# Performance work log

Hardware: AMD Instinct MI355X
Metric: run time of the kernel (lower is better)

## Reference

```python
import math
import jax, jax.numpy as jnp
import numpy as np

B, T, C, H = 2, 1024, 1024, 16
D = C // H
BASE_SCALE = 0.03125
ATTN_ALPHA_INIT, MLP_ALPHA_INIT = 0.05, 0.05


def sinusoidal_embeddings(n, d):
    pos = jnp.arange(n, dtype=jnp.float32)[:, None]
    div = jnp.exp(jnp.arange(0, d, 2, dtype=jnp.float32) * (-math.log(10000.0) / d))
    emb = jnp.zeros((n, d), dtype=jnp.float32)
    emb = emb.at[:, 0::2].set(jnp.sin(pos * div))
    emb = emb.at[:, 1::2].set(jnp.cos(pos * div))
    return emb


def apply_rope(pos, q):
    # pos: (T, D); q: (B, H, T, D). Faithful to source: returns only the rotated-scaled component.
    pos = pos[-q.shape[2]:]
    d = q.shape[-1]
    sin, cos = pos[:, : d // 2], pos[:, d // 2 :]
    q_rot = jnp.stack((-q[..., 1::2], q[..., ::2]), axis=-1)  # (B,H,T,D/2,2)
    sc = jnp.stack((cos, sin), axis=-1)  # (T, D/2, 2)
    return (q_rot * sc).reshape(q.shape)


def justnorm(x):
    return x / jnp.linalg.norm(x, axis=-1, keepdims=True)


def setup_inputs() -> dict:
    key = jax.random.key(0)
    ks = jax.random.split(key, 14)
    w = lambda k, shape: jax.random.normal(k, shape, jnp.float32) * 0.02
    return {
        "h": jax.random.normal(ks[0], (B, T, C), jnp.float32),
        "Wq": w(ks[1], (C, C)),
        "Wk": w(ks[2], (C, C)),
        "Wv": w(ks[3], (C, C)),
        "Wo": w(ks[4], (C, C)),
        "Wfc": w(ks[5], (8 * C, C)),
        "Wproj": w(ks[6], (C, 4 * C)),
        "sqk": BASE_SCALE * jnp.ones(C) + w(ks[7], (C,)) * 0.05,
        "suv": jnp.ones(8 * C) + w(ks[8], (8 * C,)) * 0.05,
        "attn_alpha": BASE_SCALE * jnp.ones(C) + w(ks[9], (C,)) * 0.05,
        "mlp_alpha": BASE_SCALE * jnp.ones(C) + w(ks[10], (C,)) * 0.05,
        "thr_c": 1.6 * jnp.ones(H) + w(ks[11], (H,)) * 0.5,
        "stp": 10.0 * jnp.ones(H),
    }


def reference(h, Wq, Wk, Wv, Wo, Wfc, Wproj, sqk, suv, attn_alpha, mlp_alpha, thr_c, stp):
    softmax_scale = math.sqrt(D)  # nGPT uses sqrt(head_dim) since q,k are unit-normalized

    # --- attention branch (no pre-norm in nGPT mode) ---
    q = (h @ Wq.T).reshape(B, T, H, D).transpose(0, 2, 1, 3)  # (B,H,T,D)
    k = (h @ Wk.T).reshape(B, T, H, D).transpose(0, 2, 1, 3)
    v = (h @ Wv.T).reshape(B, T, H, D).transpose(0, 2, 1, 3)

    pos = sinusoidal_embeddings(T, D)
    q = apply_rope(pos, q)
    k = apply_rope(pos, k)

    sqk_s = (sqk * (1.0 / BASE_SCALE)).reshape(1, H, 1, D)
    q = sqk_s * justnorm(q)
    k = sqk_s * justnorm(k)

    scores = jnp.einsum("bhqd,bhkd->bhqk", q, k) * softmax_scale  # (B,H,T,T)
    causal = jnp.tril(jnp.ones((T, T), dtype=bool))
    w = jax.nn.softmax(jnp.where(causal, scores, -1e9), axis=-1)
    # soft score threshold: per-head sigmoid gate on raw scores, then renormalize
    gate = jax.nn.sigmoid(stp[None, :, None, None] * (scores - thr_c[None, :, None, None]))
    w = w * gate
    w = w / jnp.sum(w, axis=-1, keepdims=True)

    y = jnp.einsum("bhqk,bhkd->bhqd", w, v).transpose(0, 2, 1, 3).reshape(B, T, C)
    h_att = y @ Wo.T

    lr = jnp.abs(attn_alpha * (ATTN_ALPHA_INIT / BASE_SCALE))
    A = justnorm(h)
    Bn = justnorm(h_att)
    h = justnorm(A + lr * (Bn - A))

    # --- MLP branch ---
    uv = h @ Wfc.T  # (B,T,8C)
    uv = (suv * math.sqrt(C)) * uv
    u, vv = jnp.split(uv, 2, axis=-1)
    x_mlp = u * (vv * jax.nn.sigmoid(vv))
    h_mlp = x_mlp @ Wproj.T

    lr2 = jnp.abs(mlp_alpha * (MLP_ALPHA_INIT / BASE_SCALE))
    A = justnorm(h)
    Bn = justnorm(h_mlp)
    h = justnorm(A + lr2 * (Bn - A))
    return h
```

## Files before the change

kernel.cpp:

```cpp
#include <hip/hip_runtime.h>
#include <hip/hip_bf16.h>
#include <math.h>

typedef _Float16 f16x8 __attribute__((ext_vector_type(8)));
typedef float f32x4 __attribute__((ext_vector_type(4)));
typedef float f32x2 __attribute__((ext_vector_type(2)));
typedef unsigned short u16;
typedef unsigned int u32;
typedef u16 u16x4 __attribute__((ext_vector_type(4)));
typedef u16 u16x8 __attribute__((ext_vector_type(8)));

#define DEVI static __device__ __forceinline__
#define LDSS 72
#define MB (1u << 20)

DEVI u16 f2h(float f) {
    _Float16 h = (_Float16)f;
    return __builtin_bit_cast(u16, h);
}
DEVI float h2f(u16 u) {
    return (float)__builtin_bit_cast(_Float16, u);
}
DEVI f32x4 mfma16(f16x8 a, f16x8 b, f32x4 c) {
    return __builtin_amdgcn_mfma_f32_16x16x32_f16(a, b, c, 0, 0, 0);
}
DEVI void gload16(const u16* g, u16* l) {
    __builtin_amdgcn_global_load_lds((const __attribute__((address_space(1))) void*)g,
                                     (__attribute__((address_space(3))) void*)l, 16, 0, 0);
}

DEVI void stage128(const u16* __restrict__ g, size_t row0, int ldg, int k0, u16* lds) {
    int t = threadIdx.x;
    const u16* src = g + (row0 + (size_t)(t >> 3)) * (size_t)ldg + k0 + (t & 7) * 8;
    u16* dst = lds + (t >> 6) * 512;
#pragma unroll
    for (int is = 0; is < 4; is++)
        gload16(src + (size_t)is * 32 * ldg, dst + is * 2048);
}

DEVI void gemm128_core(const u16* __restrict__ A, const u16* __restrict__ B,
                       int ldk, int kbeg, int kend, int m0, int n0,
                       u16* As, u16* Bs, f32x4 acc[4][4]) {
    int lane = threadIdx.x & 63, w = threadIdx.x >> 6;
    int wm = (w >> 1) * 64, wn = (w & 1) * 64;
    int lrow = lane & 15, lg = lane >> 4;
    for (int k0 = kbeg; k0 < kend; k0 += 64) {
        __syncthreads();
        stage128(A, m0, ldk, k0, As);
        stage128(B, n0, ldk, k0, Bs);
        __syncthreads();
#pragma unroll
        for (int ks = 0; ks < 2; ks++) {
            f16x8 af[4], bf[4];
#pragma unroll
            for (int i = 0; i < 4; i++) {
                af[i] = *reinterpret_cast<f16x8*>(&As[(wm + i * 16 + lrow) * 64 + ks * 32 + lg * 8]);
                bf[i] = *reinterpret_cast<f16x8*>(&Bs[(wn + i * 16 + lrow) * 64 + ks * 32 + lg * 8]);
            }
#pragma unroll
            for (int i = 0; i < 4; i++)
#pragma unroll
                for (int j = 0; j < 4; j++)
                    acc[i][j] = mfma16(af[i], bf[j], acc[i][j]);
        }
    }
}

__global__ void cvt_kernel(const float* __restrict__ h, const float* __restrict__ Wq,
                           const float* __restrict__ Wk, const float* __restrict__ Wv,
                           const float* __restrict__ Wo, const float* __restrict__ Wfc,
                           const float* __restrict__ Wproj, u16* __restrict__ dst) {
    int bid = blockIdx.x;
    const float* src;
    size_t doff;
    int sb;
    if (bid < 1024)      { src = h;     sb = 0;    doff = 0; }
    else if (bid < 1536) { src = Wq;    sb = 1024; doff = 2097152; }
    else if (bid < 2048) { src = Wk;    sb = 1536; doff = 3145728; }
    else if (bid < 2560) { src = Wv;    sb = 2048; doff = 4194304; }
    else if (bid < 3072) { src = Wo;    sb = 2560; doff = 5242880; }
    else if (bid < 7168) { src = Wfc;   sb = 3072; doff = 10485760; }
    else                 { src = Wproj; sb = 7168; doff = 6291456; }
    size_t idx = (size_t)(bid - sb) * 2048 + threadIdx.x * 8;
    f32x4 a = *reinterpret_cast<const f32x4*>(src + idx);
    f32x4 b = *reinterpret_cast<const f32x4*>(src + idx + 4);
    u16x8 o;
    o[0] = f2h(a[0]); o[1] = f2h(a[1]); o[2] = f2h(a[2]); o[3] = f2h(a[3]);
    o[4] = f2h(b[0]); o[5] = f2h(b[1]); o[6] = f2h(b[2]); o[7] = f2h(b[3]);
    *reinterpret_cast<u16x8*>(dst + doff + idx) = o;
}

__global__ __launch_bounds__(256, 2) void qkv_h_kernel(
    const u16* __restrict__ hb, const u16* __restrict__ Wqh, const u16* __restrict__ Wkh,
    const u16* __restrict__ Wvh, u16* __restrict__ qb, u16* __restrict__ kb, u16* __restrict__ vb) {
    __shared__ u16 As[128 * 64];
    __shared__ u16 Bs[128 * 64];
    int z = blockIdx.z;
    const u16* W = (z == 0) ? Wqh : (z == 1) ? Wkh : Wvh;
    u16* dst = (z == 0) ? qb : (z == 1) ? kb : vb;
    int m0 = blockIdx.y * 128, n0 = blockIdx.x * 128;
    f32x4 acc[4][4];
    f32x4 zf = {0.f, 0.f, 0.f, 0.f};
#pragma unroll
    for (int i = 0; i < 4; i++)
#pragma unroll
        for (int j = 0; j < 4; j++) acc[i][j] = zf;
    gemm128_core(hb, W, 1024, 0, 1024, m0, n0, As, Bs, acc);
    int lane = threadIdx.x & 63, w = threadIdx.x >> 6;
    int wm = (w >> 1) * 64, wn = (w & 1) * 64;
    int lrow = lane & 15, lg = lane >> 4;
#pragma unroll
    for (int i = 0; i < 4; i++)
#pragma unroll
        for (int j = 0; j < 4; j++)
#pragma unroll
            for (int r = 0; r < 4; r++) {
                int m = m0 + wm + i * 16 + lg * 4 + r;
                int n = n0 + wn + j * 16 + lrow;
                dst[(size_t)m * 1024 + n] = f2h(acc[i][j][r]);
            }
}

__global__ __launch_bounds__(256, 2) void gemm_h_kernel(
    const u16* __restrict__ A, const u16* __restrict__ B, u16* __restrict__ out,
    int ldk, int ksplit, int osplit, int N) {
    __shared__ u16 As[128 * 64];
    __shared__ u16 Bs[128 * 64];
    int z = blockIdx.z;
    int m0 = blockIdx.y * 128, n0 = blockIdx.x * 128;
    f32x4 acc[4][4];
    f32x4 zf = {0.f, 0.f, 0.f, 0.f};
#pragma unroll
    for (int i = 0; i < 4; i++)
#pragma unroll
        for (int j = 0; j < 4; j++) acc[i][j] = zf;
    gemm128_core(A, B, ldk, z * ksplit, (z + 1) * ksplit, m0, n0, As, Bs, acc);
    u16* o = out + (size_t)z * osplit;
    int lane = threadIdx.x & 63, w = threadIdx.x >> 6;
    int wm = (w >> 1) * 64, wn = (w & 1) * 64;
    int lrow = lane & 15, lg = lane >> 4;
#pragma unroll
    for (int i = 0; i < 4; i++)
#pragma unroll
        for (int j = 0; j < 4; j++)
#pragma unroll
            for (int r = 0; r < 4; r++) {
                int m = m0 + wm + i * 16 + lg * 4 + r;
                int n = n0 + wn + j * 16 + lrow;
                o[(size_t)m * N + n] = f2h(acc[i][j][r]);
            }
}

__global__ void qkprep_kernel(u16* __restrict__ qb, u16* __restrict__ kb,
                              const float* __restrict__ sqk) {
    u16* buf = blockIdx.z ? kb : qb;
    int pair = blockIdx.x * 4 + (threadIdx.x >> 6);
    int m = pair >> 4, hh = pair & 15;
    int tt = m & 1023;
    int d = threadIdx.x & 63;
    size_t off = (size_t)m * 1024 + hh * 64 + d;
    float x = h2f(buf[off]);
    float xn = __shfl_xor(x, 1);
    int j = (d & 1) ? ((d - 1) >> 1) : (32 + (d >> 1));
    float dv = exp2f(-(float)(j >> 1) * 0.41524101186092029f);
    float ang = (float)tt * dv;
    float e = (j & 1) ? cosf(ang) : sinf(ang);
    float xr = (d & 1) ? (xn * e) : (-xn * e);
    float ss = xr * xr;
#pragma unroll
    for (int o = 1; o < 64; o <<= 1) ss += __shfl_xor(ss, o);
    float sc = rsqrtf(ss) * sqk[hh * 64 + d] * 32.0f;
    buf[off] = f2h(xr * sc);
}

__global__ __launch_bounds__(128) void attn_kernel(
    const u16* __restrict__ qb, const u16* __restrict__ kb, const u16* __restrict__ vb,
    const float* __restrict__ thr_c, const float* __restrict__ stp,
    u16* __restrict__ yph, f32x2* __restrict__ mden) {
    const int T = 1024, C = 1024;
    int qt = 31 - (blockIdx.x >> 2);
    int c = blockIdx.x & 3;
    int bh = blockIdx.y;
    int b = bh >> 4, hh = bh & 15;
    int q0 = qt * 32;
    int nkt = (q0 >> 6) + 1;
    __shared__ u16 Vt[2][64 * LDSS];
    __shared__ u16 Ps[32 * LDSS];
    int t = threadIdx.x;
    int lane = t & 63, w = t >> 6;
    int lrow = lane & 15, lg = lane >> 4, lk = lg * 8;
    int kvp = t & 31, db = t >> 5;

    const u16* qrowp = qb + (size_t)(b * T + q0 + w * 16 + lrow) * C + hh * 64;
    f16x8 qfr[2];
    qfr[0] = *reinterpret_cast<const f16x8*>(qrowp + lk);
    qfr[1] = *reinterpret_cast<const f16x8*>(qrowp + 32 + lk);

    float thr = thr_c[hh], st = stp[hh];
    float stthr = st * thr;
    float mrun = -1e30f, den = 0.f;
    f32x4 yacc[4];
    f32x4 zf = {0.f, 0.f, 0.f, 0.f};
#pragma unroll
    for (int i = 0; i < 4; i++) yacc[i] = zf;
    int qg = q0 + w * 16 + lrow;

    f16x8 kpre[8];
    u16x4 vr[8];
    const u16* kbase0 = kb + (size_t)(b * T + lrow) * C + hh * 64 + lk;
    const u16* vbase0 = vb + (size_t)(b * T + 2 * kvp) * C + hh * 64 + db * 16;

    if (c < nkt) {
        const u16* kbase = kbase0 + (size_t)(c << 6) * C;
        const u16* vsrc = vbase0 + (size_t)(c << 6) * C;
#pragma unroll
        for (int ks = 0; ks < 2; ks++)
#pragma unroll
            for (int f = 0; f < 4; f++)
                kpre[ks * 4 + f] = *reinterpret_cast<const f16x8*>(kbase + (size_t)(f * 16) * C + ks * 32);
#pragma unroll
        for (int dd = 0; dd < 4; dd++) {
            vr[dd * 2] = *reinterpret_cast<const u16x4*>(vsrc + dd * 4);
            vr[dd * 2 + 1] = *reinterpret_cast<const u16x4*>(vsrc + C + dd * 4);
        }
    }

    int bufsel = 0;
    for (int kt = c; kt < nkt; kt += 4) {
        int kv0 = kt << 6;
        u16* VB = Vt[bufsel];
        bufsel ^= 1;
#pragma unroll
        for (int dd = 0; dd < 4; dd++)
#pragma unroll
            for (int e = 0; e < 4; e++) {
                u32 v = (u32)vr[dd * 2][e] | ((u32)vr[dd * 2 + 1][e] << 16);
                *reinterpret_cast<u32*>(&VB[(db * 16 + dd * 4 + e) * LDSS + 2 * kvp]) = v;
            }
        f32x4 sacc[4];
#pragma unroll
        for (int f = 0; f < 4; f++) sacc[f] = zf;
#pragma unroll
        for (int ks = 0; ks < 2; ks++)
#pragma unroll
            for (int f = 0; f < 4; f++)
                sacc[f] = mfma16(kpre[ks * 4 + f], qfr[ks], sacc[f]);

        if (kt + 4 < nkt) {
            const u16* kbase = kbase0 + (size_t)((kt + 4) << 6) * C;
            const u16* vsrc = vbase0 + (size_t)((kt + 4) << 6) * C;
#pragma unroll
            for (int ks = 0; ks < 2; ks++)
#pragma unroll
                for (int f = 0; f < 4; f++)
                    kpre[ks * 4 + f] = *reinterpret_cast<const f16x8*>(kbase + (size_t)(f * 16) * C + ks * 32);
#pragma unroll
            for (int dd = 0; dd < 4; dd++) {
                vr[dd * 2] = *reinterpret_cast<const u16x4*>(vsrc + dd * 4);
                vr[dd * 2 + 1] = *reinterpret_cast<const u16x4*>(vsrc + C + dd * 4);
            }
        }

        float svv[16];
        float tmax = -1e30f;
        bool last = (kt == nkt - 1);
#pragma unroll
        for (int f = 0; f < 4; f++)
#pragma unroll
            for (int r = 0; r < 4; r++) {
                float s = sacc[f][r] * 8.0f;
                if (last) {
                    int kvg = kv0 + f * 16 + lg * 4 + r;
                    if (kvg > qg) s = -1e30f;
                }
                svv[f * 4 + r] = s;
                tmax = fmaxf(tmax, s);
            }
        tmax = fmaxf(tmax, __shfl_xor(tmax, 16));
        tmax = fmaxf(tmax, __shfl_xor(tmax, 32));
        float zM = stthr - st * tmax;
        float spM = tmax - __logf(1.0f + __expf(zM));
        float mnew = fmaxf(mrun, spM);
        float alpha = __expf(mrun - mnew);
        float tden = 0.f;
        u16 pu[16];
#pragma unroll
        for (int i = 0; i < 16; i++) {
            float s = svv[i];
            float e2 = __expf(s - mnew);
            float eg = __expf(stthr - st * s);
            float p = e2 * __builtin_amdgcn_rcpf(1.0f + eg);
            u16 ph = f2h(p);
            pu[i] = ph;
            tden += h2f(ph);
        }
        tden += __shfl_xor(tden, 16);
        tden += __shfl_xor(tden, 32);
        den = den * alpha + tden;
        mrun = mnew;

#pragma unroll
        for (int f = 0; f < 4; f++) {
            u16x4 u = {pu[f * 4 + 0], pu[f * 4 + 1], pu[f * 4 + 2], pu[f * 4 + 3]};
            *reinterpret_cast<u16x4*>(&Ps[(w * 16 + lrow) * LDSS + f * 16 + lg * 4]) = u;
        }
        float a4[4];
#pragma unroll
        for (int r = 0; r < 4; r++) a4[r] = __shfl(alpha, lg * 4 + r);
#pragma unroll
        for (int nf = 0; nf < 4; nf++)
#pragma unroll
            for (int r = 0; r < 4; r++) yacc[nf][r] *= a4[r];

        __syncthreads();

#pragma unroll
        for (int ks = 0; ks < 2; ks++) {
            f16x8 pf = *reinterpret_cast<f16x8*>(&Ps[(w * 16 + lrow) * LDSS + ks * 32 + lk]);
#pragma unroll
            for (int nf = 0; nf < 4; nf++) {
                f16x8 vf = *reinterpret_cast<f16x8*>(&VB[(nf * 16 + lrow) * LDSS + ks * 32 + lk]);
                yacc[nf] = mfma16(pf, vf, yacc[nf]);
            }
        }
    }
    u16* ypc = yph + (size_t)c * 2097152;
#pragma unroll
    for (int nf = 0; nf < 4; nf++)
#pragma unroll
        for (int r = 0; r < 4; r++) {
            int qrow = q0 + w * 16 + lg * 4 + r;
            ypc[(size_t)(b * T + qrow) * C + hh * 64 + nf * 16 + lrow] = f2h(yacc[nf][r]);
        }
    if (lg == 0) {
        f32x2 md;
        md[0] = mrun; md[1] = den;
        mden[((size_t)c * 32 + bh) * 1024 + (q0 + w * 16 + lrow)] = md;
    }
}

__global__ void attn_merge_kernel(const u16* __restrict__ yph, const f32x2* __restrict__ mden,
                                  u16* __restrict__ y) {
    int row = blockIdx.x;
    int b = row >> 10, tr = row & 1023;
    int t = threadIdx.x;
#pragma unroll
    for (int i = 0; i < 4; i++) {
        int idx = t + 256 * i;
        int hh = idx >> 6;
        float m[4], d[4];
        float M = -1e30f;
#pragma unroll
        for (int p = 0; p < 4; p++) {
            f32x2 md = mden[((size_t)p * 32 + b * 16 + hh) * 1024 + tr];
            m[p] = md[0]; d[p] = md[1];
            M = fmaxf(M, m[p]);
        }
        size_t off = (size_t)row * 1024 + idx;
        float dn = 0.f, acc = 0.f;
#pragma unroll
        for (int p = 0; p < 4; p++) {
            float wp = __expf(m[p] - M);
            dn += d[p] * wp;
            acc += h2f(yph[off + (size_t)p * 2097152]) * wp;
        }
        y[off] = f2h(acc / dn);
    }
}

__global__ __launch_bounds__(256, 2) void fc_silu_kernel(
    const u16* __restrict__ h1h, const u16* __restrict__ Wfch,
    const float* __restrict__ suv, u16* __restrict__ xmlp) {
    __shared__ u16 As[128 * 64];
    __shared__ u16 Bu[128 * 64];
    __shared__ u16 Bv[128 * 64];
    int m0 = blockIdx.y * 128, n0 = blockIdx.x * 128;
    f32x4 au[4][4], av[4][4];
    f32x4 zf = {0.f, 0.f, 0.f, 0.f};
#pragma unroll
    for (int i = 0; i < 4; i++)
#pragma unroll
        for (int j = 0; j < 4; j++) { au[i][j] = zf; av[i][j] = zf; }
    int lane = threadIdx.x & 63, w = threadIdx.x >> 6;
    int wm = (w >> 1) * 64, wn = (w & 1) * 64;
    int lrow = lane & 15, lg = lane >> 4;
    for (int k0 = 0; k0 < 1024; k0 += 64) {
        __syncthreads();
        stage128(h1h, m0, 1024, k0, As);
        stage128(Wfch, n0, 1024, k0, Bu);
        stage128(Wfch, 4096 + n0, 1024, k0, Bv);
        __syncthreads();
#pragma unroll
        for (int ks = 0; ks < 2; ks++) {
            f16x8 af[4], bu[4], bv[4];
#pragma unroll
            for (int i = 0; i < 4; i++) {
                af[i] = *reinterpret_cast<f16x8*>(&As[(wm + i * 16 + lrow) * 64 + ks * 32 + lg * 8]);
                bu[i] = *reinterpret_cast<f16x8*>(&Bu[(wn + i * 16 + lrow) * 64 + ks * 32 + lg * 8]);
                bv[i] = *reinterpret_cast<f16x8*>(&Bv[(wn + i * 16 + lrow) * 64 + ks * 32 + lg * 8]);
            }
#pragma unroll
            for (int i = 0; i < 4; i++)
#pragma unroll
                for (int j = 0; j < 4; j++) {
                    au[i][j] = mfma16(af[i], bu[j], au[i][j]);
                    av[i][j] = mfma16(af[i], bv[j], av[i][j]);
                }
        }
    }
#pragma unroll
    for (int i = 0; i < 4; i++)
#pragma unroll
        for (int j = 0; j < 4; j++) {
            int n = n0 + wn + j * 16 + lrow;
            float su = suv[n] * 32.0f;
            float sv = suv[4096 + n] * 32.0f;
#pragma unroll
            for (int r = 0; r < 4; r++) {
                int m = m0 + wm + i * 16 + lg * 4 + r;
                float uu = au[i][j][r] * su;
                float vv = av[i][j][r] * sv;
                float sig = 1.0f / (1.0f + __expf(-vv));
                xmlp[(size_t)m * 4096 + n] = f2h(uu * vv * sig);
            }
        }
}

__global__ void normres_kernel(const float* __restrict__ base, const u16* __restrict__ dparts,
                               int nparts, int pstride, const float* __restrict__ alpha,
                               float* __restrict__ outf, u16* __restrict__ outh) {
    int row = blockIdx.x;
    int t = threadIdx.x;
    const float* pb = base + (size_t)row * 1024;
    float xb[4], xd[4];
    float ssb = 0.f, ssd = 0.f;
#pragma unroll
    for (int i = 0; i < 4; i++) {
        size_t off = (size_t)row * 1024 + t + 256 * i;
        xb[i] = pb[t + 256 * i];
        float d = 0.f;
        for (int p = 0; p < nparts; p++) d += h2f(dparts[off + (size_t)p * pstride]);
        xd[i] = d;
        ssb += xb[i] * xb[i];
        ssd += xd[i] * xd[i];
    }
#pragma unroll
    for (int o = 1; o < 64; o <<= 1) { ssb += __shfl_xor(ssb, o); ssd += __shfl_xor(ssd, o); }
    __shared__ float red[8];
    int w = t >> 6;
    if ((t & 63) == 0) { red[w * 2] = ssb; red[w * 2 + 1] = ssd; }
    __syncthreads();
    ssb = red[0] + red[2] + red[4] + red[6];
    ssd = red[1] + red[3] + red[5] + red[7];
    float rb = rsqrtf(ssb), rd = rsqrtf(ssd);
    float c[4];
    float ssc = 0.f;
#pragma unroll
    for (int i = 0; i < 4; i++) {
        float a = xb[i] * rb;
        float bb = xd[i] * rd;
        float lr = fabsf(alpha[t + 256 * i] * 1.6f);
        float cv = a + lr * (bb - a);
        c[i] = cv;
        ssc += cv * cv;
    }
#pragma unroll
    for (int o = 1; o < 64; o <<= 1) ssc += __shfl_xor(ssc, o);
    __syncthreads();
    if ((t & 63) == 0) red[w] = ssc;
    __syncthreads();
    ssc = red[0] + red[1] + red[2] + red[3];
    float rc = rsqrtf(ssc);
#pragma unroll
    for (int i = 0; i < 4; i++) {
        float v = c[i] * rc;
        size_t off = (size_t)row * 1024 + t + 256 * i;
        outf[off] = v;
        if (outh) outh[off] = f2h(v);
    }
}

extern "C" void kernel_launch(void* const* d_in, const int* in_sizes, int n_in,
                              void* d_out, int out_size, void* d_ws, size_t ws_size,
                              hipStream_t stream) {
    const float* h = (const float*)d_in[0];
    const float* Wq = (const float*)d_in[1];
    const float* Wk = (const float*)d_in[2];
    const float* Wv = (const float*)d_in[3];
    const float* Wo = (const float*)d_in[4];
    const float* Wfc = (const float*)d_in[5];
    const float* Wproj = (const float*)d_in[6];
    const float* sqk = (const float*)d_in[7];
    const float* suv = (const float*)d_in[8];
    const float* attn_alpha = (const float*)d_in[9];
    const float* mlp_alpha = (const float*)d_in[10];
    const float* thr_c = (const float*)d_in[11];
    const float* stp = (const float*)d_in[12];

    char* ws = (char*)d_ws;
    u16* f16heap = (u16*)ws;
    u16* hb     = f16heap + 0;
    u16* Wqh    = f16heap + 2097152;
    u16* Wkh    = f16heap + 3145728;
    u16* Wvh    = f16heap + 4194304;
    u16* Woh    = f16heap + 5242880;
    u16* Wprojh = f16heap + 6291456;
    u16* Wfch   = f16heap + 10485760;
    u16* partsP = Wfch;
    u16* qb   = (u16*)(ws + (size_t)36 * MB);
    u16* kb   = (u16*)(ws + (size_t)40 * MB);
    u16* vb   = (u16*)(ws + (size_t)44 * MB);
    u16* y    = (u16*)(ws + (size_t)48 * MB);
    u16* yph  = (u16*)(ws + (size_t)52 * MB);
    f32x2* mden = (f32x2*)(ws + (size_t)68 * MB);
    u16* hattP = (u16*)(ws + (size_t)52 * MB);
    float* h1 = (float*)(ws + (size_t)36 * MB);
    u16* h1h  = (u16*)(ws + (size_t)44 * MB);
    u16* xmlp = (u16*)(ws + (size_t)52 * MB);
    float* out = (float*)d_out;

    cvt_kernel<<<9216, 256, 0, stream>>>(h, Wq, Wk, Wv, Wo, Wfc, Wproj, f16heap);
    qkv_h_kernel<<<dim3(8, 16, 3), 256, 0, stream>>>(hb, Wqh, Wkh, Wvh, qb, kb, vb);
    qkprep_kernel<<<dim3(8192, 1, 2), 256, 0, stream>>>(qb, kb, sqk);
    attn_kernel<<<dim3(128, 32), 128, 0, stream>>>(qb, kb, vb, thr_c, stp, yph, mden);
    attn_merge_kernel<<<2048, 256, 0, stream>>>(yph, mden, y);
    gemm_h_kernel<<<dim3(8, 16, 4), 256, 0, stream>>>(y, Woh, hattP, 1024, 256, 2097152, 1024);
    normres_kernel<<<2048, 256, 0, stream>>>(h, hattP, 4, 2097152, attn_alpha, h1, h1h);
    fc_silu_kernel<<<dim3(32, 16), 256, 0, stream>>>(h1h, Wfch, suv, xmlp);
    gemm_h_kernel<<<dim3(8, 16, 4), 256, 0, stream>>>(xmlp, Wprojh, partsP, 4096, 1024, 2097152, 1024);
    normres_kernel<<<2048, 256, 0, stream>>>(h1, partsP, 4, 2097152, mlp_alpha, out, (u16*)nullptr);
}
```

Measured before the change: 203.5 us.

## Double-buffer GEMM LDS staging and interleave Wfc rows for fc_silu

Replaces the single-buffer GEMM mainloop with a double-buffered one that issues the next K-tile's global-to-LDS loads before computing the current tile, using vmcnt waits and raw barriers. The Wfc conversion now interleaves u and v rows, so fc_silu can use the shared GEMM core with a 128-wide tile and pair the u/v accumulators via a lane shuffle. This doubles the fc_silu grid and drops its separate triple-buffer loop. The cost is twice the LDS per block, which may lower occupancy. It also relies on hand-written waitcnt values being correct.

```diff
diff --git a/kernel.cpp b/kernel.cpp
--- a/kernel.cpp
+++ b/kernel.cpp
@@ -38,24 +38,36 @@
         gload16(src + (size_t)is * 32 * ldg, dst + is * 2048);
 }
 
-DEVI void gemm128_core(const u16* __restrict__ A, const u16* __restrict__ B,
+DEVI void gemm128_dbuf(const u16* __restrict__ A, const u16* __restrict__ B,
                        int ldk, int kbeg, int kend, int m0, int n0,
-                       u16* As, u16* Bs, f32x4 acc[4][4]) {
+                       u16* As0, u16* As1, u16* Bs0, u16* Bs1, f32x4 acc[4][4]) {
     int lane = threadIdx.x & 63, w = threadIdx.x >> 6;
     int wm = (w >> 1) * 64, wn = (w & 1) * 64;
     int lrow = lane & 15, lg = lane >> 4;
-    for (int k0 = kbeg; k0 < kend; k0 += 64) {
-        __syncthreads();
-        stage128(A, m0, ldk, k0, As);
-        stage128(B, n0, ldk, k0, Bs);
-        __syncthreads();
+    int nt = (kend - kbeg) >> 6;
+    stage128(A, m0, ldk, kbeg, As0);
+    stage128(B, n0, ldk, kbeg, Bs0);
+    for (int t = 0; t < nt; t++) {
+        u16* Ac = (t & 1) ? As1 : As0;
+        u16* Bc = (t & 1) ? Bs1 : Bs0;
+        if (t + 1 < nt) {
+            u16* An = (t & 1) ? As0 : As1;
+            u16* Bn = (t & 1) ? Bs0 : Bs1;
+            stage128(A, m0, ldk, kbeg + (t + 1) * 64, An);
+            stage128(B, n0, ldk, kbeg + (t + 1) * 64, Bn);
+            asm volatile("s_waitcnt vmcnt(8)" ::: "memory");
+        } else {
+            asm volatile("s_waitcnt vmcnt(0)" ::: "memory");
+        }
+        __builtin_amdgcn_s_barrier();
+        __builtin_amdgcn_sched_barrier(0);
 #pragma unroll
         for (int ks = 0; ks < 2; ks++) {
             f16x8 af[4], bf[4];
 #pragma unroll
             for (int i = 0; i < 4; i++) {
-                af[i] = *reinterpret_cast<f16x8*>(&As[(wm + i * 16 + lrow) * 64 + ks * 32 + lg * 8]);
-                bf[i] = *reinterpret_cast<f16x8*>(&Bs[(wn + i * 16 + lrow) * 64 + ks * 32 + lg * 8]);
+                af[i] = *reinterpret_cast<f16x8*>(&Ac[(wm + i * 16 + lrow) * 64 + ks * 32 + lg * 8]);
+                bf[i] = *reinterpret_cast<f16x8*>(&Bc[(wn + i * 16 + lrow) * 64 + ks * 32 + lg * 8]);
             }
 #pragma unroll
             for (int i = 0; i < 4; i++)
@@ -63,6 +75,7 @@
                 for (int j = 0; j < 4; j++)
                     acc[i][j] = mfma16(af[i], bf[j], acc[i][j]);
         }
+        __builtin_amdgcn_s_barrier();
     }
 }
 
@@ -74,12 +87,13 @@
     const float* src;
     size_t doff;
     int sb;
+    bool ilv = false;
     if (bid < 1024)      { src = h;     sb = 0;    doff = 0; }
     else if (bid < 1536) { src = Wq;    sb = 1024; doff = 2097152; }
     else if (bid < 2048) { src = Wk;    sb = 1536; doff = 3145728; }
     else if (bid < 2560) { src = Wv;    sb = 2048; doff = 4194304; }
     else if (bid < 3072) { src = Wo;    sb = 2560; doff = 5242880; }
-    else if (bid < 7168) { src = Wfc;   sb = 3072; doff = 10485760; }
+    else if (bid < 7168) { src = Wfc;   sb = 3072; doff = 10485760; ilv = true; }
     else                 { src = Wproj; sb = 7168; doff = 6291456; }
     size_t idx = (size_t)(bid - sb) * 2048 + threadIdx.x * 8;
     f32x4 a = *reinterpret_cast<const f32x4*>(src + idx);
@@ -87,14 +101,20 @@
     u16x8 o;
     o[0] = f2h(a[0]); o[1] = f2h(a[1]); o[2] = f2h(a[2]); o[3] = f2h(a[3]);
     o[4] = f2h(b[0]); o[5] = f2h(b[1]); o[6] = f2h(b[2]); o[7] = f2h(b[3]);
-    *reinterpret_cast<u16x8*>(dst + doff + idx) = o;
+    size_t didx = idx;
+    if (ilv) {
+        size_t row = idx >> 10, col = idx & 1023;
+        size_t nrow = (row < 4096) ? (row * 2) : ((row - 4096) * 2 + 1);
+        didx = nrow * 1024 + col;
+    }
+    *reinterpret_cast<u16x8*>(dst + doff + didx) = o;
 }
 
 __global__ __launch_bounds__(256, 2) void qkv_h_kernel(
     const u16* __restrict__ hb, const u16* __restrict__ Wqh, const u16* __restrict__ Wkh,
     const u16* __restrict__ Wvh, u16* __restrict__ qb, u16* __restrict__ kb, u16* __restrict__ vb) {
-    __shared__ u16 As[128 * 64];
-    __shared__ u16 Bs[128 * 64];
+    __shared__ u16 As[2][128 * 64];
+    __shared__ u16 Bs[2][128 * 64];
     int z = blockIdx.z;
     const u16* W = (z == 0) ? Wqh : (z == 1) ? Wkh : Wvh;
     u16* dst = (z == 0) ? qb : (z == 1) ? kb : vb;
@@ -105,7 +125,7 @@
     for (int i = 0; i < 4; i++)
 #pragma unroll
         for (int j = 0; j < 4; j++) acc[i][j] = zf;
-    gemm128_core(hb, W, 1024, 0, 1024, m0, n0, As, Bs, acc);
+    gemm128_dbuf(hb, W, 1024, 0, 1024, m0, n0, As[0], As[1], Bs[0], Bs[1], acc);
     int lane = threadIdx.x & 63, w = threadIdx.x >> 6;
     int wm = (w >> 1) * 64, wn = (w & 1) * 64;
     int lrow = lane & 15, lg = lane >> 4;
@@ -124,8 +144,8 @@
 __global__ __launch_bounds__(256, 2) void gemm_h_kernel(
     const u16* __restrict__ A, const u16* __restrict__ B, u16* __restrict__ out,
     int ldk, int ksplit, int osplit, int N) {
-    __shared__ u16 As[128 * 64];
-    __shared__ u16 Bs[128 * 64];
+    __shared__ u16 As[2][128 * 64];
+    __shared__ u16 Bs[2][128 * 64];
     int z = blockIdx.z;
     int m0 = blockIdx.y * 128, n0 = blockIdx.x * 128;
     f32x4 acc[4][4];
@@ -134,7 +154,7 @@
     for (int i = 0; i < 4; i++)
 #pragma unroll
         for (int j = 0; j < 4; j++) acc[i][j] = zf;
-    gemm128_core(A, B, ldk, z * ksplit, (z + 1) * ksplit, m0, n0, As, Bs, acc);
+    gemm128_dbuf(A, B, ldk, z * ksplit, (z + 1) * ksplit, m0, n0, As[0], As[1], Bs[0], Bs[1], acc);
     u16* o = out + (size_t)z * osplit;
     int lane = threadIdx.x & 63, w = threadIdx.x >> 6;
     int wm = (w >> 1) * 64, wn = (w & 1) * 64;
@@ -369,59 +389,41 @@
 }
 
 __global__ __launch_bounds__(256, 2) void fc_silu_kernel(
-    const u16* __restrict__ h1h, const u16* __restrict__ Wfch,
+    const u16* __restrict__ h1h, const u16* __restrict__ Wfc2,
     const float* __restrict__ suv, u16* __restrict__ xmlp) {
-    __shared__ u16 As[128 * 64];
-    __shared__ u16 Bu[128 * 64];
-    __shared__ u16 Bv[128 * 64];
-    int m0 = blockIdx.y * 128, n0 = blockIdx.x * 128;
-    f32x4 au[4][4], av[4][4];
+    __shared__ u16 As[2][128 * 64];
+    __shared__ u16 Bs[2][128 * 64];
+    int m0 = blockIdx.y * 128, n0 = blockIdx.x * 64;
+    f32x4 acc[4][4];
     f32x4 zf = {0.f, 0.f, 0.f, 0.f};
 #pragma unroll
     for (int i = 0; i < 4; i++)
 #pragma unroll
-        for (int j = 0; j < 4; j++) { au[i][j] = zf; av[i][j] = zf; }
+        for (int j = 0; j < 4; j++) acc[i][j] = zf;
+    gemm128_dbuf(h1h, Wfc2, 1024, 0, 1024, m0, 2 * n0, As[0], As[1], Bs[0], Bs[1], acc);
     int lane = threadIdx.x & 63, w = threadIdx.x >> 6;
     int wm = (w >> 1) * 64, wn = (w & 1) * 64;
     int lrow = lane & 15, lg = lane >> 4;
-    for (int k0 = 0; k0 < 1024; k0 += 64) {
-        __syncthreads();
-        stage128(h1h, m0, 1024, k0, As);
-        stage128(Wfch, n0, 1024, k0, Bu);
-        stage128(Wfch, 4096 + n0, 1024, k0, Bv);
-        __syncthreads();
-#pragma unroll
-        for (int ks = 0; ks < 2; ks++) {
-            f16x8 af[4], bu[4], bv[4];
-#pragma unroll
-            for (int i = 0; i < 4; i++) {
-                af[i] = *reinterpret_cast<f16x8*>(&As[(wm + i * 16 + lrow) * 64 + ks * 32 + lg * 8]);
-                bu[i] = *reinterpret_cast<f16x8*>(&Bu[(wn + i * 16 + lrow) * 64 + ks * 32 + lg * 8]);
-                bv[i] = *reinterpret_cast<f16x8*>(&Bv[(wn + i * 16 + lrow) * 64 + ks * 32 + lg * 8]);
-            }
-#pragma unroll
-            for (int i = 0; i < 4; i++)
-#pragma unroll
-                for (int j = 0; j < 4; j++) {
-                    au[i][j] = mfma16(af[i], bu[j], au[i][j]);
-                    av[i][j] = mfma16(af[i], bv[j], av[i][j]);
-                }
-        }
-    }
 #pragma unroll
     for (int i = 0; i < 4; i++)
 #pragma unroll
         for (int j = 0; j < 4; j++) {
-            int n = n0 + wn + j * 16 + lrow;
+            int bn = wn + j * 16 + lrow;
+            int n = n0 + (bn >> 1);
+            bool isu = (bn & 1) == 0;
             float su = suv[n] * 32.0f;
             float sv = suv[4096 + n] * 32.0f;
 #pragma unroll
             for (int r = 0; r < 4; r++) {
-                int m = m0 + wm + i * 16 + lg * 4 + r;
-                float uu = au[i][j][r] * su;
-                float vv = av[i][j][r] * sv;
+                float own = acc[i][j][r];
+                float other = __shfl_xor(own, 1);
+                float uu = (isu ? own : other) * su;
+                float vv = (isu ? other : own) * sv;
                 float sig = 1.0f / (1.0f + __expf(-vv));
-                xmlp[(size_t)m * 4096 + n] = f2h(uu * vv * sig);
+                if (isu) {
+                    int m = m0 + wm + i * 16 + lg * 4 + r;
+                    xmlp[(size_t)m * 4096 + n] = f2h(uu * vv * sig);
+                }
             }
         }
 }
@@ -505,8 +507,8 @@
     u16* Wvh    = f16heap + 4194304;
     u16* Woh    = f16heap + 5242880;
     u16* Wprojh = f16heap + 6291456;
-    u16* Wfch   = f16heap + 10485760;
-    u16* partsP = Wfch;
+    u16* Wfc2   = f16heap + 10485760;
+    u16* partsP = Wfc2;
     u16* qb   = (u16*)(ws + (size_t)36 * MB);
     u16* kb   = (u16*)(ws + (size_t)40 * MB);
     u16* vb   = (u16*)(ws + (size_t)44 * MB);
@@ -526,7 +528,7 @@
     attn_merge_kernel<<<2048, 256, 0, stream>>>(yph, mden, y);
     gemm_h_kernel<<<dim3(8, 16, 4), 256, 0, stream>>>(y, Woh, hattP, 1024, 256, 2097152, 1024);
     normres_kernel<<<2048, 256, 0, stream>>>(h, hattP, 4, 2097152, attn_alpha, h1, h1h);
-    fc_silu_kernel<<<dim3(32, 16), 256, 0, stream>>>(h1h, Wfch, suv, xmlp);
+    fc_silu_kernel<<<dim3(64, 16), 256, 0, stream>>>(h1h, Wfc2, suv, xmlp);
     gemm_h_kernel<<<dim3(8, 16, 4), 256, 0, stream>>>(xmlp, Wprojh, partsP, 4096, 1024, 2097152, 1024);
     normres_kernel<<<2048, 256, 0, stream>>>(h1, partsP, 4, 2097152, mlp_alpha, out, (u16*)nullptr);
 }
```

Result: slower. 221.5 us (+8.8%).

## Fuse RoPE and QK normalization into QKV GEMM epilogue; raise MFMA priority

Applied to the files above, without the earlier changes.

Moves the rotary embedding and per-head L2 normalization with sqk scaling into the epilogue of the QKV projection GEMM. Each wave owns a 64-wide head slice, so the per-row sum of squares is reduced across lanes with shuffles inside the wave. This drops the separate qkprep kernel, its extra read and write of the q and k buffers, and one launch. It also wraps the attention MFMA sections in s_setprio to favor the matrix-issue phases, at the cost of more transcendental work in the GEMM epilogue.

```diff
diff --git a/kernel.cpp b/kernel.cpp
--- a/kernel.cpp
+++ b/kernel.cpp
@@ -92,7 +92,8 @@
 
 __global__ __launch_bounds__(256, 2) void qkv_h_kernel(
     const u16* __restrict__ hb, const u16* __restrict__ Wqh, const u16* __restrict__ Wkh,
-    const u16* __restrict__ Wvh, u16* __restrict__ qb, u16* __restrict__ kb, u16* __restrict__ vb) {
+    const u16* __restrict__ Wvh, const float* __restrict__ sqk,
+    u16* __restrict__ qb, u16* __restrict__ kb, u16* __restrict__ vb) {
     __shared__ u16 As[128 * 64];
     __shared__ u16 Bs[128 * 64];
     int z = blockIdx.z;
@@ -109,16 +110,53 @@
     int lane = threadIdx.x & 63, w = threadIdx.x >> 6;
     int wm = (w >> 1) * 64, wn = (w & 1) * 64;
     int lrow = lane & 15, lg = lane >> 4;
-#pragma unroll
-    for (int i = 0; i < 4; i++)
-#pragma unroll
-        for (int j = 0; j < 4; j++)
+    if (z == 2) {
+#pragma unroll
+        for (int i = 0; i < 4; i++)
+#pragma unroll
+            for (int j = 0; j < 4; j++)
+#pragma unroll
+                for (int r = 0; r < 4; r++) {
+                    int m = m0 + wm + i * 16 + lg * 4 + r;
+                    int n = n0 + wn + j * 16 + lrow;
+                    dst[(size_t)m * 1024 + n] = f2h(acc[i][j][r]);
+                }
+    } else {
+        int hh64 = ((n0 + wn) >> 6) * 64;
+#pragma unroll
+        for (int i = 0; i < 4; i++)
 #pragma unroll
             for (int r = 0; r < 4; r++) {
                 int m = m0 + wm + i * 16 + lg * 4 + r;
-                int n = n0 + wn + j * 16 + lrow;
-                dst[(size_t)m * 1024 + n] = f2h(acc[i][j][r]);
-            }
+                int tt = m & 1023;
+                float xr[4];
+                float ss = 0.f;
+#pragma unroll
+                for (int j = 0; j < 4; j++) {
+                    float x = acc[i][j][r];
+                    float xn = __shfl_xor(x, 1);
+                    int d = j * 16 + lrow;
+                    int jj = (d & 1) ? ((d - 1) >> 1) : (32 + (d >> 1));
+                    float dv = exp2f(-(float)(jj >> 1) * 0.41524101186092029f);
+                    float ang = (float)tt * dv;
+                    float e = (jj & 1) ? cosf(ang) : sinf(ang);
+                    float v = (d & 1) ? (xn * e) : (-xn * e);
+                    xr[j] = v;
+                    ss += v * v;
+                }
+                ss += __shfl_xor(ss, 1);
+                ss += __shfl_xor(ss, 2);
+                ss += __shfl_xor(ss, 4);
+                ss += __shfl_xor(ss, 8);
+                float rs = rsqrtf(ss) * 32.0f;
+#pragma unroll
+                for (int j = 0; j < 4; j++) {
+                    int d = j * 16 + lrow;
+                    int n = n0 + wn + j * 16 + lrow;
+                    dst[(size_t)m * 1024 + n] = f2h(xr[j] * rs * sqk[hh64 + d]);
+                }
+            }
+    }
 }
 
 __global__ __launch_bounds__(256, 2) void gemm_h_kernel(
@@ -149,28 +187,6 @@
                 int n = n0 + wn + j * 16 + lrow;
                 o[(size_t)m * N + n] = f2h(acc[i][j][r]);
             }
-}
-
-__global__ void qkprep_kernel(u16* __restrict__ qb, u16* __restrict__ kb,
-                              const float* __restrict__ sqk) {
-    u16* buf = blockIdx.z ? kb : qb;
-    int pair = blockIdx.x * 4 + (threadIdx.x >> 6);
-    int m = pair >> 4, hh = pair & 15;
-    int tt = m & 1023;
-    int d = threadIdx.x & 63;
-    size_t off = (size_t)m * 1024 + hh * 64 + d;
-    float x = h2f(buf[off]);
-    float xn = __shfl_xor(x, 1);
-    int j = (d & 1) ? ((d - 1) >> 1) : (32 + (d >> 1));
-    float dv = exp2f(-(float)(j >> 1) * 0.41524101186092029f);
-    float ang = (float)tt * dv;
-    float e = (j & 1) ? cosf(ang) : sinf(ang);
-    float xr = (d & 1) ? (xn * e) : (-xn * e);
-    float ss = xr * xr;
-#pragma unroll
-    for (int o = 1; o < 64; o <<= 1) ss += __shfl_xor(ss, o);
-    float sc = rsqrtf(ss) * sqk[hh * 64 + d] * 32.0f;
-    buf[off] = f2h(xr * sc);
 }
 
 __global__ __launch_bounds__(128) void attn_kernel(
@@ -240,11 +256,13 @@
         f32x4 sacc[4];
 #pragma unroll
         for (int f = 0; f < 4; f++) sacc[f] = zf;
+        __builtin_amdgcn_s_setprio(1);
 #pragma unroll
         for (int ks = 0; ks < 2; ks++)
 #pragma unroll
             for (int f = 0; f < 4; f++)
                 sacc[f] = mfma16(kpre[ks * 4 + f], qfr[ks], sacc[f]);
+        __builtin_amdgcn_s_setprio(0);
 
         if (kt + 4 < nkt) {
             const u16* kbase = kbase0 + (size_t)((kt + 4) << 6) * C;
@@ -314,6 +332,7 @@
 
         __syncthreads();
 
+        __builtin_amdgcn_s_setprio(1);
 #pragma unroll
         for (int ks = 0; ks < 2; ks++) {
             f16x8 pf = *reinterpret_cast<f16x8*>(&Ps[(w * 16 + lrow) * LDSS + ks * 32 + lk]);
@@ -323,6 +342,7 @@
                 yacc[nf] = mfma16(pf, vf, yacc[nf]);
             }
         }
+        __builtin_amdgcn_s_setprio(0);
     }
     u16* ypc = yph + (size_t)c * 2097152;
 #pragma unroll
@@ -520,8 +540,7 @@
     float* out = (float*)d_out;
 
     cvt_kernel<<<9216, 256, 0, stream>>>(h, Wq, Wk, Wv, Wo, Wfc, Wproj, f16heap);
-    qkv_h_kernel<<<dim3(8, 16, 3), 256, 0, stream>>>(hb, Wqh, Wkh, Wvh, qb, kb, vb);
-    qkprep_kernel<<<dim3(8192, 1, 2), 256, 0, stream>>>(qb, kb, sqk);
+    qkv_h_kernel<<<dim3(8, 16, 3), 256, 0, stream>>>(hb, Wqh, Wkh, Wvh, sqk, qb, kb, vb);
     attn_kernel<<<dim3(128, 32), 128, 0, stream>>>(qb, kb, vb, thr_c, stp, yph, mden);
     attn_merge_kernel<<<2048, 256, 0, stream>>>(yph, mden, y);
     gemm_h_kernel<<<dim3(8, 16, 4), 256, 0, stream>>>(y, Woh, hattP, 1024, 256, 2097152, 1024);
```

Result: slower. 260.2 us (+27.9%).
